# Performance work log

Hardware: AMD Instinct MI355X
Metric: run time of the kernel (lower is better)

## Reference

```python
import jax, jax.numpy as jnp
import numpy as np


def setup_inputs() -> dict:
    key = jax.random.key(0)
    k1, k2 = jax.random.split(key)
    N, K, D = 262144, 1024, 256
    z_e = jax.random.normal(k1, (N, D), dtype=jnp.float32)
    # torch init: uniform(-1/num_embeddings, 1/num_embeddings)
    codebook = jax.random.uniform(k2, (K, D), dtype=jnp.float32,
                                  minval=-1.0 / K, maxval=1.0 / K)
    return {"z_e": z_e, "codebook": codebook}


def reference(z_e, codebook):
    # distances: ||z||^2 + ||c||^2 - 2 z c^T  -> [N, K]
    distances = (jnp.sum(z_e ** 2, axis=1, keepdims=True)
                 + jnp.sum(codebook ** 2, axis=1)
                 - 2.0 * jnp.matmul(z_e, codebook.T))
    min_encoding_indices = jnp.argmin(distances, axis=1)[:, None]  # [N, 1]
    z_q = codebook[min_encoding_indices[:, 0]]  # [N, D]

    # loss_vq = mse(z_q.detach(), z_e)
    loss_vq = jnp.mean((jax.lax.stop_gradient(z_q) - z_e) ** 2)

    # loss_mean = mse(z_e, mean_codebook.detach())
    mean_codebook = jnp.mean(codebook, axis=0)  # [D]
    loss_mean = jnp.mean((z_e - jax.lax.stop_gradient(mean_codebook)) ** 2)

    # straight-through estimator
    z_q_st = z_e + jax.lax.stop_gradient(z_q - z_e)
    return (z_q_st, loss_vq, loss_mean, min_encoding_indices)
```

## Files before the change

### kernel.cpp

```cpp
#include <hip/hip_runtime.h>


#define NROWS 262144
#define KCODES 1024
#define DDIM 256
#define ND ((size_t)NROWS * (size_t)DDIM)
#define M1F 6e-4f

typedef unsigned int uint;
typedef _Float16 f16x8 __attribute__((ext_vector_type(8)));
typedef float f32x4v __attribute__((ext_vector_type(4)));

__device__ inline float fadd(float a, float b) {
    float d; asm("v_add_f32 %0, %1, %2" : "=v"(d) : "v"(a), "v"(b)); return d;
}
__device__ inline float fmul(float a, float b) {
    float d; asm("v_mul_f32 %0, %1, %2" : "=v"(d) : "v"(a), "v"(b)); return d;
}
__device__ inline float fsub(float a, float b) {
    float d; asm("v_sub_f32 %0, %1, %2" : "=v"(d) : "v"(a), "v"(b)); return d;
}
__device__ inline float ffma(float a, float b, float c) {
    float d; asm("v_fma_f32 %0, %1, %2, %3" : "=v"(d) : "v"(a), "v"(b), "v"(c)); return d;
}

__device__ float np_sq_sum256(const float* __restrict__ a) {
    float tot[2];
    #pragma unroll 1
    for (int h = 0; h < 2; ++h) {
        const float* p = a + h * 128;
        float r[8];
        #pragma unroll
        for (int j = 0; j < 8; ++j) r[j] = fmul(p[j], p[j]);
        #pragma unroll 1
        for (int i = 8; i < 128; i += 8)
            #pragma unroll
            for (int j = 0; j < 8; ++j) r[j] = fadd(r[j], fmul(p[i + j], p[i + j]));
        tot[h] = fadd(fadd(fadd(r[0], r[1]), fadd(r[2], r[3])),
                      fadd(fadd(r[4], r[5]), fadd(r[6], r[7])));
    }
    return fadd(tot[0], tot[1]);
}

__device__ float blas_dot256(const float* __restrict__ zr, const float* __restrict__ cr) {
    float dot = 0.f;
    #pragma unroll 4
    for (int d4 = 0; d4 < 64; ++d4) {
        float4 zz = *(const float4*)(zr + d4 * 4);
        float4 cc = *(const float4*)(cr + d4 * 4);
        dot = ffma(zz.x, cc.x, dot); dot = ffma(zz.y, cc.y, dot);
        dot = ffma(zz.z, cc.z, dot); dot = ffma(zz.w, cc.w, dot);
    }
    return dot;
}

__global__ void k_prep(const float* __restrict__ cb, char* __restrict__ cbh,
                       float* __restrict__ scp, float* __restrict__ mAcc) {
    int bx = blockIdx.x;
    if (bx < 128) {
        int g = bx * 256 + threadIdx.x;
        int t = g >> 10, c = (g >> 5) & 31, j = g & 31;
        const float* s = cb + (size_t)(t * 32 + c) * DDIM + j * 8;
        float4 v0 = *(const float4*)s, v1 = *(const float4*)(s + 4);
        f16x8 h;
        h[0] = (_Float16)(v0.x * 1024.f); h[1] = (_Float16)(v0.y * 1024.f);
        h[2] = (_Float16)(v0.z * 1024.f); h[3] = (_Float16)(v0.w * 1024.f);
        h[4] = (_Float16)(v1.x * 1024.f); h[5] = (_Float16)(v1.y * 1024.f);
        h[6] = (_Float16)(v1.z * 1024.f); h[7] = (_Float16)(v1.w * 1024.f);
        uint byte = (uint)(c * 512 + j * 16) ^ (uint)((c & 7) << 4);
        *(f16x8*)(cbh + (size_t)t * 16384 + byte) = h;
    } else if (bx < 132) {
        int code = (bx - 128) * 256 + threadIdx.x;
        if (code < KCODES) scp[code] = np_sq_sum256(cb + (size_t)code * DDIM);
    } else {
        int d = threadIdx.x;
        int b = bx - 132;
        float s = 0.f;
        for (int i = 0; i < 64; ++i) s += cb[(size_t)(b * 64 + i) * DDIM + d];
        atomicAdd(&mAcc[d], s);
    }
}

__global__ void k_meanfin(const float* __restrict__ mAcc,
                          float* __restrict__ mvec, double* __restrict__ M2p) {
    __shared__ double red[256];
    int d = threadIdx.x;
    float m = mAcc[d] * (1.0f / 1024.0f);
    mvec[d] = m;
    red[d] = (double)m * (double)m;
    __syncthreads();
    for (int off = 128; off; off >>= 1) {
        if (d < off) red[d] += red[d + off];
        __syncthreads();
    }
    if (d == 0) *M2p = red[0];
}

#define GLOAD_LDS16(g, l) \
    __builtin_amdgcn_global_load_lds( \
        (const __attribute__((address_space(1))) void*)(g), \
        (__attribute__((address_space(3))) void*)(l), 16, 0, 0)

__launch_bounds__(256, 3)
__global__ void k_main(const float* __restrict__ z, const char* __restrict__ cbh,
                       const float* __restrict__ sc, const float* __restrict__ mvec,
                       float* __restrict__ out, uint* __restrict__ counts,
                       uint2* __restrict__ listTri, uint* __restrict__ listFull,
                       int capTri, int capFull,
                       double* __restrict__ lossA, double* __restrict__ lossB) {
    __shared__ char tiles[2][16384] __attribute__((aligned(16)));
    __shared__ float sc_lds[1024];
    __shared__ float statA[128], statZM[128];
    __shared__ float lred[2];

    const int tid = threadIdx.x;
    const int wave = tid >> 6;
    const int lane = tid & 63;
    const int l15 = lane & 15;
    const int lg = lane >> 4;
    const int blockRow = blockIdx.x * 128;

    if (tid < 2) lred[tid] = 0.f;
    for (int i = tid; i < 1024; i += 256) sc_lds[i] = sc[i];

    f16x8 za[2][8];
    #pragma unroll
    for (int m = 0; m < 2; ++m) {
        const float* zr = z + (size_t)(blockRow + wave * 32 + m * 16 + l15) * DDIM;
        float a2 = 0.f, zm = 0.f;
        #pragma unroll
        for (int kk = 0; kk < 8; ++kk) {
            int d0 = kk * 32 + lg * 8;
            float4 v0 = *(const float4*)(zr + d0);
            float4 v1 = *(const float4*)(zr + d0 + 4);
            float4 w0 = *(const float4*)(mvec + d0);
            float4 w1 = *(const float4*)(mvec + d0 + 4);
            a2 += v0.x * v0.x + v0.y * v0.y + v0.z * v0.z + v0.w * v0.w;
            a2 += v1.x * v1.x + v1.y * v1.y + v1.z * v1.z + v1.w * v1.w;
            zm += v0.x * w0.x + v0.y * w0.y + v0.z * w0.z + v0.w * w0.w;
            zm += v1.x * w1.x + v1.y * w1.y + v1.z * w1.z + v1.w * w1.w;
            f16x8 h;
            h[0] = (_Float16)v0.x; h[1] = (_Float16)v0.y;
            h[2] = (_Float16)v0.z; h[3] = (_Float16)v0.w;
            h[4] = (_Float16)v1.x; h[5] = (_Float16)v1.y;
            h[6] = (_Float16)v1.z; h[7] = (_Float16)v1.w;
            za[m][kk] = h;
        }
        a2 += __shfl_xor(a2, 16); a2 += __shfl_xor(a2, 32);
        zm += __shfl_xor(zm, 16); zm += __shfl_xor(zm, 32);
        if (lg == 0) {
            statA[wave * 32 + m * 16 + l15] = a2;
            statZM[wave * 32 + m * 16 + l15] = zm;
        }
    }
    __syncthreads();

    float k1v[2][2][4], k2v[2][2][4], k3v[2][2][4];
    #pragma unroll
    for (int n = 0; n < 2; ++n)
        #pragma unroll
        for (int m = 0; m < 2; ++m)
            #pragma unroll
            for (int r = 0; r < 4; ++r) {
                k1v[n][m][r] = 3e38f; k2v[n][m][r] = 3e38f; k3v[n][m][r] = 3e38f;
            }

    const char* gsrc0 = cbh + (size_t)wave * 4096 + (size_t)lane * 16;
    #define STAGE(T, BUF) { \
        const char* g_ = gsrc0 + (size_t)(T) * 16384; \
        char* l_ = &tiles[BUF][wave * 4096]; \
        _Pragma("unroll") \
        for (int i_ = 0; i_ < 4; ++i_) GLOAD_LDS16(g_ + i_ * 1024, l_ + i_ * 1024); \
    }

    #define COMPUTE(T, BUF) { \
        f32x4v acc[2][2]; \
        _Pragma("unroll") \
        for (int m = 0; m < 2; ++m) \
            _Pragma("unroll") \
            for (int n = 0; n < 2; ++n) acc[m][n] = (f32x4v){0.f, 0.f, 0.f, 0.f}; \
        const char* tb = &tiles[BUF][0]; \
        _Pragma("unroll") \
        for (int kk = 0; kk < 8; ++kk) { \
            _Pragma("unroll") \
            for (int n = 0; n < 2; ++n) { \
                int lcode = n * 16 + l15; \
                uint byte = (uint)(lcode * 512 + kk * 64 + lg * 16) ^ (uint)((lcode & 7) << 4); \
                f16x8 b = *(const f16x8*)(tb + byte); \
                acc[0][n] = __builtin_amdgcn_mfma_f32_16x16x32_f16(za[0][kk], b, acc[0][n], 0, 0, 0); \
                acc[1][n] = __builtin_amdgcn_mfma_f32_16x16x32_f16(za[1][kk], b, acc[1][n], 0, 0, 0); \
            } \
        } \
        int tbase = (T) * 32; \
        _Pragma("unroll") \
        for (int n = 0; n < 2; ++n) { \
            int codev = tbase + n * 16 + l15; \
            float scv = sc_lds[codev]; \
            _Pragma("unroll") \
            for (int m = 0; m < 2; ++m) \
                _Pragma("unroll") \
                for (int r = 0; r < 4; ++r) { \
                    float s = fmaf(acc[m][n][r], -0.001953125f, scv); \
                    uint kb = (__float_as_uint(s) & 0xFFFFFC00u) | (uint)codev; \
                    float k = __uint_as_float(kb); \
                    float o1 = k1v[n][m][r], o2 = k2v[n][m][r]; \
                    k3v[n][m][r] = __builtin_amdgcn_fmed3f(o2, k3v[n][m][r], k); \
                    k2v[n][m][r] = __builtin_amdgcn_fmed3f(o1, o2, k); \
                    k1v[n][m][r] = fminf(o1, k); \
                } \
        } \
    }

    STAGE(0, 0);
    #pragma unroll 1
    for (int t = 0; t < 31; ++t) {
        STAGE(t + 1, (t + 1) & 1);
        __syncthreads();
        COMPUTE(t, t & 1);
        __syncthreads();
    }
    __syncthreads();
    COMPUTE(31, 1);

    float lA = 0.f, lB = 0.f;
    #pragma unroll
    for (int m = 0; m < 2; ++m)
        #pragma unroll
        for (int r = 0; r < 4; ++r) {
            float x1 = k1v[0][m][r], x2 = k2v[0][m][r], x3 = k3v[0][m][r];
            float y1 = k1v[1][m][r], y2 = k2v[1][m][r], y3 = k3v[1][m][r];
            float mx = fmaxf(x1, y1);
            float a3 = fminf(fminf(__builtin_amdgcn_fmed3f(x2, y2, mx), x3), y3);
            float a2 = fminf(fminf(mx, x2), y2);
            float a1 = fminf(x1, y1);
            #pragma unroll
            for (int mk = 1; mk <= 8; mk <<= 1) {
                float b1 = __shfl_xor(a1, mk);
                float b2 = __shfl_xor(a2, mk);
                float b3 = __shfl_xor(a3, mk);
                float mx2 = fmaxf(a1, b1);
                float n3 = fminf(fminf(__builtin_amdgcn_fmed3f(a2, b2, mx2), a3), b3);
                float n2 = fminf(fminf(mx2, a2), b2);
                a1 = fminf(a1, b1); a2 = n2; a3 = n3;
            }
            if (l15 == 0) {
                int rowL = wave * 32 + m * 16 + lg * 4 + r;
                int row = blockRow + rowL;
                int i1 = (int)(__float_as_uint(a1) & 1023u);
                int i2 = (int)(__float_as_uint(a2) & 1023u);
                int i3 = (int)(__float_as_uint(a3) & 1023u);
                int flag = (a3 - a1 < M1F) ? 2 : ((a2 - a1 < M1F) ? 1 : 0);
                float slotval = (float)i1;
                if (flag == 2) {
                    uint p = atomicAdd(&counts[1], 1u);
                    if (p < (uint)capFull) listFull[p] = (uint)row;
                    else slotval = (float)(i1 | (1 << 20));
                } else if (flag == 1) {
                    uint p = atomicAdd(&counts[0], 1u);
                    if (p < (uint)capTri)
                        listTri[p] = make_uint2((uint)row, (uint)(i1 | (i2 << 10) | (i3 << 20)));
                    else slotval = (float)(i1 | (1 << 20));
                }
                out[ND + 2 + (size_t)row] = slotval;
                lA += statA[rowL] + a1;
                lB += statA[rowL] - 2.f * statZM[rowL];
            }
        }
    if (l15 == 0) { atomicAdd(&lred[0], lA); atomicAdd(&lred[1], lB); }
    __syncthreads();
    if (tid == 0) {
        atomicAdd(lossA, (double)lred[0]);
        atomicAdd(lossB, (double)lred[1]);
    }
}

__global__ void k_gather(const float* __restrict__ cb, float* __restrict__ out) {
    __shared__ int idx[128];
    const int tid = threadIdx.x;
    const int blockRow = blockIdx.x * 128;
    if (tid < 128) idx[tid] = ((int)out[ND + 2 + (size_t)(blockRow + tid)]) & 1023;
    __syncthreads();
    float4* out4 = (float4*)out;
    const float4* cb4 = (const float4*)cb;
    #pragma unroll 4
    for (int i = 0; i < 32; ++i) {
        int q = i * 256 + tid;
        int rowL = q >> 6, ch = q & 63;
        int code = idx[rowL];
        out4[(size_t)(blockRow + rowL) * 64 + ch] = cb4[(size_t)code * 64 + ch];
    }
}

__launch_bounds__(256)
__global__ void k_refine_tri(const float* __restrict__ z, const float* __restrict__ cb,
                             const float* __restrict__ scp,
                             const uint* __restrict__ counts,
                             const uint2* __restrict__ listTri, int capTri,
                             float* __restrict__ out) {
    __shared__ float B[4][4][256];
    const int wv = threadIdx.x >> 6;
    const int lane = threadIdx.x & 63;
    uint n = counts[0];
    if (n > (uint)capTri) n = (uint)capTri;
    uint nw = gridDim.x * 4;
    for (uint it = blockIdx.x * 4 + wv; it < n; it += nw) {
        uint2 e = listTri[it];
        int row = (int)e.x;
        int i1 = (int)(e.y & 1023), i2 = (int)((e.y >> 10) & 1023), i3 = (int)((e.y >> 20) & 1023);
        *(float4*)&B[wv][0][lane * 4] = *(const float4*)(z + (size_t)row * DDIM + lane * 4);
        *(float4*)&B[wv][1][lane * 4] = *(const float4*)(cb + (size_t)i1 * DDIM + lane * 4);
        *(float4*)&B[wv][2][lane * 4] = *(const float4*)(cb + (size_t)i2 * DDIM + lane * 4);
        *(float4*)&B[wv][3][lane * 4] = *(const float4*)(cb + (size_t)i3 * DDIM + lane * 4);
        asm volatile("s_waitcnt vmcnt(0) lgkmcnt(0)" ::: "memory");
        __builtin_amdgcn_sched_barrier(0);
        float A = np_sq_sum256(B[wv][0]);
        float dA = 0.f, dB = 0.f, dC = 0.f;
        #pragma unroll 4
        for (int d4 = 0; d4 < 64; ++d4) {
            float4 zz = *(const float4*)&B[wv][0][d4 * 4];
            float4 ca = *(const float4*)&B[wv][1][d4 * 4];
            float4 cc = *(const float4*)&B[wv][2][d4 * 4];
            float4 cd = *(const float4*)&B[wv][3][d4 * 4];
            dA = ffma(zz.x, ca.x, dA); dA = ffma(zz.y, ca.y, dA);
            dA = ffma(zz.z, ca.z, dA); dA = ffma(zz.w, ca.w, dA);
            dB = ffma(zz.x, cc.x, dB); dB = ffma(zz.y, cc.y, dB);
            dB = ffma(zz.z, cc.z, dB); dB = ffma(zz.w, cc.w, dB);
            dC = ffma(zz.x, cd.x, dC); dC = ffma(zz.y, cd.y, dC);
            dC = ffma(zz.z, cd.z, dC); dC = ffma(zz.w, cd.w, dC);
        }
        float d1 = fsub(fadd(A, scp[i1]), fmul(2.f, dA));
        float d2 = fsub(fadd(A, scp[i2]), fmul(2.f, dB));
        float d3 = fsub(fadd(A, scp[i3]), fmul(2.f, dC));
        int win = i1; float bd = d1;
        if (d2 < bd || (d2 == bd && i2 < win)) { bd = d2; win = i2; }
        if (d3 < bd || (d3 == bd && i3 < win)) { bd = d3; win = i3; }
        if (win != i1) {
            if (lane == 0) out[ND + 2 + (size_t)row] = (float)win;
            *(float4*)(out + (size_t)row * DDIM + lane * 4) =
                *(const float4*)(cb + (size_t)win * DDIM + lane * 4);
        }
    }
}

__launch_bounds__(256, 2)
__global__ void k_refine_full(const float* __restrict__ z, const float* __restrict__ cb,
                              const float* __restrict__ scp,
                              const uint* __restrict__ counts,
                              const uint* __restrict__ listFull, int capFull,
                              float* __restrict__ out) {
    __shared__ float zrow[256];
    __shared__ float avs[256];
    __shared__ int ais[256];
    __shared__ int winsh;

    uint n = counts[1];
    if (n > (uint)capFull) n = (uint)capFull;
    const int tid = threadIdx.x;

    for (uint j = blockIdx.x; j < n; j += gridDim.x) {
        int row = (int)listFull[j];
        __syncthreads();
        if (tid < 64)
            *(float4*)&zrow[tid * 4] = *(const float4*)(z + (size_t)row * DDIM + tid * 4);
        __syncthreads();

        float A = np_sq_sum256(zrow);

        float d0 = 0.f, d1 = 0.f, d2 = 0.f, d3 = 0.f;
        const float* c0 = cb + (size_t)(tid + 0) * DDIM;
        const float* c1 = cb + (size_t)(tid + 256) * DDIM;
        const float* c2 = cb + (size_t)(tid + 512) * DDIM;
        const float* c3 = cb + (size_t)(tid + 768) * DDIM;
        #pragma unroll 4
        for (int q = 0; q < 64; ++q) {
            float4 zz = *(const float4*)&zrow[q * 4];
            float4 a = *(const float4*)(c0 + q * 4);
            float4 b = *(const float4*)(c1 + q * 4);
            float4 c = *(const float4*)(c2 + q * 4);
            float4 d = *(const float4*)(c3 + q * 4);
            d0 = ffma(zz.x, a.x, d0); d0 = ffma(zz.y, a.y, d0);
            d0 = ffma(zz.z, a.z, d0); d0 = ffma(zz.w, a.w, d0);
            d1 = ffma(zz.x, b.x, d1); d1 = ffma(zz.y, b.y, d1);
            d1 = ffma(zz.z, b.z, d1); d1 = ffma(zz.w, b.w, d1);
            d2 = ffma(zz.x, c.x, d2); d2 = ffma(zz.y, c.y, d2);
            d2 = ffma(zz.z, c.z, d2); d2 = ffma(zz.w, c.w, d2);
            d3 = ffma(zz.x, d.x, d3); d3 = ffma(zz.y, d.y, d3);
            d3 = ffma(zz.z, d.z, d3); d3 = ffma(zz.w, d.w, d3);
        }
        float best = 1e30f; int bi = 0x7fffffff;
        float dd[4] = {d0, d1, d2, d3};
        #pragma unroll
        for (int kk = 0; kk < 4; ++kk) {
            int code = tid + kk * 256;
            float dist = fsub(fadd(A, scp[code]), fmul(2.f, dd[kk]));
            if (dist < best || (dist == best && code < bi)) { best = dist; bi = code; }
        }
        avs[tid] = best; ais[tid] = bi;
        __syncthreads();
        for (int off = 128; off; off >>= 1) {
            if (tid < off) {
                float o = avs[tid + off]; int oi = ais[tid + off];
                if (o < avs[tid] || (o == avs[tid] && oi < ais[tid])) {
                    avs[tid] = o; ais[tid] = oi;
                }
            }
            __syncthreads();
        }
        if (tid == 0) {
            winsh = ais[0];
            out[ND + 2 + (size_t)row] = (float)ais[0];
        }
        __syncthreads();
        int win = winsh;
        out[(size_t)row * DDIM + tid] = cb[(size_t)win * DDIM + tid];
    }
}

__global__ void k_sweep(const float* __restrict__ z, const float* __restrict__ cb,
                        const float* __restrict__ scp, float* __restrict__ out) {
    int row = blockIdx.x * 256 + threadIdx.x;
    float v = out[ND + 2 + (size_t)row];
    if (v < 1048576.f) return;
    int enc = (int)v;
    int i1 = enc & 1023;
    const float* zr = z + (size_t)row * DDIM;
    float A = np_sq_sum256(zr);
    float best = 1e30f; int win = 0x7fffffff;
    for (int code = 0; code < KCODES; ++code) {
        float dot = blas_dot256(zr, cb + (size_t)code * DDIM);
        float dist = fsub(fadd(A, scp[code]), fmul(2.f, dot));
        if (dist < best) { best = dist; win = code; }
    }
    out[ND + 2 + (size_t)row] = (float)win;
    if (win != i1) {
        const float4* cw = (const float4*)(cb + (size_t)win * DDIM);
        float4* ow = (float4*)(out + (size_t)row * DDIM);
        for (int c = 0; c < 64; ++c) ow[c] = cw[c];
    }
}

__global__ void k_final(const double* __restrict__ lossA, const double* __restrict__ lossB,
                        const double* __restrict__ M2p, float* __restrict__ out) {
    if (threadIdx.x == 0) {
        double nd = (double)ND;
        out[ND] = (float)(*lossA / nd);
        out[ND + 1] = (float)((*lossB + (double)NROWS * (*M2p)) / nd);
    }
}

extern "C" void kernel_launch(void* const* d_in, const int* in_sizes, int n_in,
                              void* d_out, int out_size, void* d_ws, size_t ws_size,
                              hipStream_t stream) {
    const float* z = (const float*)d_in[0];
    const float* cb = (const float*)d_in[1];
    float* out = (float*)d_out;

    double* lossA = (double*)d_ws;
    double* lossB = lossA + 1;
    double* M2p   = lossA + 2;
    uint*   counts = (uint*)((char*)d_ws + 24);
    float*  mAcc  = (float*)((char*)d_ws + 32);
    float*  mvec  = (float*)((char*)d_ws + 2048);
    float*  scp   = (float*)((char*)d_ws + 4096);
    char*   cbh   = (char*)d_ws + 8192;

    size_t base = 8192 + 524288;
    size_t avail = ws_size > base ? ws_size - base : 0;
    int capFull = (int)(avail / 24);
    if (capFull > 32768) capFull = 32768;
    size_t fullBytes = ((size_t)capFull * 4 + 7) & ~(size_t)7;
    size_t availTri = avail > fullBytes ? avail - fullBytes : 0;
    int capTri = (int)(availTri / 8);
    if (capTri > 131072) capTri = 131072;

    uint*  listFull = (uint*)((char*)d_ws + base);
    uint2* listTri  = (uint2*)((char*)d_ws + base + fullBytes);

    hipMemsetAsync(d_ws, 0, 1056, stream);
    k_prep<<<148, 256, 0, stream>>>(cb, cbh, scp, mAcc);
    k_meanfin<<<1, 256, 0, stream>>>(mAcc, mvec, M2p);
    k_main<<<NROWS / 128, 256, 0, stream>>>(z, cbh, scp, mvec, out,
                                            counts, listTri, listFull,
                                            capTri, capFull, lossA, lossB);
    k_gather<<<NROWS / 128, 256, 0, stream>>>(cb, out);
    k_refine_tri<<<512, 256, 0, stream>>>(z, cb, scp, counts, listTri, capTri, out);
    k_refine_full<<<1024, 256, 0, stream>>>(z, cb, scp, counts, listFull, capFull, out);
    k_sweep<<<NROWS / 256, 256, 0, stream>>>(z, cb, scp, out);
    k_final<<<1, 64, 0, stream>>>(lossA, lossB, M2p, out);
}
```

Baseline: 965.4 us.

## Read fp16 codebook fragments directly from global memory instead of LDS staging

The codebook is now written in plain row-major fp16 instead of the swizzled tile layout. The main kernel's MFMA loop loads its B fragments straight from global memory (served by L1/L2) rather than double-buffering tiles into LDS with global_load_lds and two barriers per tile. This removes the LDS footprint and the block-wide synchronisation. In exchange, every wave issues redundant global loads with more latency exposed, and the occupancy hint drops from 3 to 2 blocks per CU.

```diff
diff --git a/kernel.cpp b/kernel.cpp
--- a/kernel.cpp
+++ b/kernel.cpp
@@ -59,16 +59,14 @@
     int bx = blockIdx.x;
     if (bx < 128) {
         int g = bx * 256 + threadIdx.x;
-        int t = g >> 10, c = (g >> 5) & 31, j = g & 31;
-        const float* s = cb + (size_t)(t * 32 + c) * DDIM + j * 8;
+        const float* s = cb + (size_t)g * 8;
         float4 v0 = *(const float4*)s, v1 = *(const float4*)(s + 4);
         f16x8 h;
         h[0] = (_Float16)(v0.x * 1024.f); h[1] = (_Float16)(v0.y * 1024.f);
         h[2] = (_Float16)(v0.z * 1024.f); h[3] = (_Float16)(v0.w * 1024.f);
         h[4] = (_Float16)(v1.x * 1024.f); h[5] = (_Float16)(v1.y * 1024.f);
         h[6] = (_Float16)(v1.z * 1024.f); h[7] = (_Float16)(v1.w * 1024.f);
-        uint byte = (uint)(c * 512 + j * 16) ^ (uint)((c & 7) << 4);
-        *(f16x8*)(cbh + (size_t)t * 16384 + byte) = h;
+        *(f16x8*)(cbh + (size_t)g * 16) = h;
     } else if (bx < 132) {
         int code = (bx - 128) * 256 + threadIdx.x;
         if (code < KCODES) scp[code] = np_sq_sum256(cb + (size_t)code * DDIM);
@@ -96,19 +94,13 @@
     if (d == 0) *M2p = red[0];
 }
 
-#define GLOAD_LDS16(g, l) \
-    __builtin_amdgcn_global_load_lds( \
-        (const __attribute__((address_space(1))) void*)(g), \
-        (__attribute__((address_space(3))) void*)(l), 16, 0, 0)
-
-__launch_bounds__(256, 3)
+__launch_bounds__(256, 2)
 __global__ void k_main(const float* __restrict__ z, const char* __restrict__ cbh,
                        const float* __restrict__ sc, const float* __restrict__ mvec,
                        float* __restrict__ out, uint* __restrict__ counts,
                        uint2* __restrict__ listTri, uint* __restrict__ listFull,
                        int capTri, int capFull,
                        double* __restrict__ lossA, double* __restrict__ lossB) {
-    __shared__ char tiles[2][16384] __attribute__((aligned(16)));
     __shared__ float sc_lds[1024];
     __shared__ float statA[128], statZM[128];
     __shared__ float lred[2];
@@ -165,62 +157,43 @@
                 k1v[n][m][r] = 3e38f; k2v[n][m][r] = 3e38f; k3v[n][m][r] = 3e38f;
             }
 
-    const char* gsrc0 = cbh + (size_t)wave * 4096 + (size_t)lane * 16;
-    #define STAGE(T, BUF) { \
-        const char* g_ = gsrc0 + (size_t)(T) * 16384; \
-        char* l_ = &tiles[BUF][wave * 4096]; \
-        _Pragma("unroll") \
-        for (int i_ = 0; i_ < 4; ++i_) GLOAD_LDS16(g_ + i_ * 1024, l_ + i_ * 1024); \
-    }
-
-    #define COMPUTE(T, BUF) { \
-        f32x4v acc[2][2]; \
-        _Pragma("unroll") \
-        for (int m = 0; m < 2; ++m) \
-            _Pragma("unroll") \
-            for (int n = 0; n < 2; ++n) acc[m][n] = (f32x4v){0.f, 0.f, 0.f, 0.f}; \
-        const char* tb = &tiles[BUF][0]; \
-        _Pragma("unroll") \
-        for (int kk = 0; kk < 8; ++kk) { \
-            _Pragma("unroll") \
-            for (int n = 0; n < 2; ++n) { \
-                int lcode = n * 16 + l15; \
-                uint byte = (uint)(lcode * 512 + kk * 64 + lg * 16) ^ (uint)((lcode & 7) << 4); \
-                f16x8 b = *(const f16x8*)(tb + byte); \
-                acc[0][n] = __builtin_amdgcn_mfma_f32_16x16x32_f16(za[0][kk], b, acc[0][n], 0, 0, 0); \
-                acc[1][n] = __builtin_amdgcn_mfma_f32_16x16x32_f16(za[1][kk], b, acc[1][n], 0, 0, 0); \
-            } \
-        } \
-        int tbase = (T) * 32; \
-        _Pragma("unroll") \
-        for (int n = 0; n < 2; ++n) { \
-            int codev = tbase + n * 16 + l15; \
-            float scv = sc_lds[codev]; \
-            _Pragma("unroll") \
-            for (int m = 0; m < 2; ++m) \
-                _Pragma("unroll") \
-                for (int r = 0; r < 4; ++r) { \
-                    float s = fmaf(acc[m][n][r], -0.001953125f, scv); \
-                    uint kb = (__float_as_uint(s) & 0xFFFFFC00u) | (uint)codev; \
-                    float k = __uint_as_float(kb); \
-                    float o1 = k1v[n][m][r], o2 = k2v[n][m][r]; \
-                    k3v[n][m][r] = __builtin_amdgcn_fmed3f(o2, k3v[n][m][r], k); \
-                    k2v[n][m][r] = __builtin_amdgcn_fmed3f(o1, o2, k); \
-                    k1v[n][m][r] = fminf(o1, k); \
-                } \
-        } \
-    }
-
-    STAGE(0, 0);
+    const char* bbase = cbh + (size_t)l15 * 512 + (size_t)lg * 16;
     #pragma unroll 1
-    for (int t = 0; t < 31; ++t) {
-        STAGE(t + 1, (t + 1) & 1);
-        __syncthreads();
-        COMPUTE(t, t & 1);
-        __syncthreads();
-    }
-    __syncthreads();
-    COMPUTE(31, 1);
+    for (int t = 0; t < 32; ++t) {
+        const char* tb = bbase + (size_t)t * 16384;
+        f32x4v acc[2][2];
+        #pragma unroll
+        for (int m = 0; m < 2; ++m)
+            #pragma unroll
+            for (int n = 0; n < 2; ++n) acc[m][n] = (f32x4v){0.f, 0.f, 0.f, 0.f};
+        #pragma unroll
+        for (int kk = 0; kk < 8; ++kk) {
+            f16x8 b0 = *(const f16x8*)(tb + kk * 64);
+            f16x8 b1 = *(const f16x8*)(tb + 8192 + kk * 64);
+            acc[0][0] = __builtin_amdgcn_mfma_f32_16x16x32_f16(za[0][kk], b0, acc[0][0], 0, 0, 0);
+            acc[1][0] = __builtin_amdgcn_mfma_f32_16x16x32_f16(za[1][kk], b0, acc[1][0], 0, 0, 0);
+            acc[0][1] = __builtin_amdgcn_mfma_f32_16x16x32_f16(za[0][kk], b1, acc[0][1], 0, 0, 0);
+            acc[1][1] = __builtin_amdgcn_mfma_f32_16x16x32_f16(za[1][kk], b1, acc[1][1], 0, 0, 0);
+        }
+        int tbase = t * 32;
+        #pragma unroll
+        for (int n = 0; n < 2; ++n) {
+            int codev = tbase + n * 16 + l15;
+            float scv = sc_lds[codev];
+            #pragma unroll
+            for (int m = 0; m < 2; ++m)
+                #pragma unroll
+                for (int r = 0; r < 4; ++r) {
+                    float s = fmaf(acc[m][n][r], -0.001953125f, scv);
+                    uint kb = (__float_as_uint(s) & 0xFFFFFC00u) | (uint)codev;
+                    float k = __uint_as_float(kb);
+                    float o1 = k1v[n][m][r], o2 = k2v[n][m][r];
+                    k3v[n][m][r] = __builtin_amdgcn_fmed3f(o2, k3v[n][m][r], k);
+                    k2v[n][m][r] = __builtin_amdgcn_fmed3f(o1, o2, k);
+                    k1v[n][m][r] = fminf(o1, k);
+                }
+        }
+    }
 
     float lA = 0.f, lB = 0.f;
     #pragma unroll
```

After: 1.225 ms. 26.9% more time.
